# Performance work log

Hardware: AMD Instinct MI355X
Metric: run time of the kernel (lower is better)

The kernel has to match this reference:

```python
import jax, jax.numpy as jnp
import numpy as np

V = 8192        # variants
NREF = 262144   # total ref reads
NALT = 131072   # total alt reads
F_READ = 11     # tensors.NUM_READ_FEATURES
F_INFO = 9      # tensors.NUM_INFO_FEATURES
H = 256         # hidden width
MAX_ALT = 10


def setup_inputs() -> dict:
    key = jax.random.key(0)
    ks = jax.random.split(key, 24)
    p = lambda k, shp: (jax.random.normal(k, shp, dtype=jnp.float32) * 0.05)
    inp = {
        "reads": jax.random.normal(ks[0], (NREF + NALT, F_READ), dtype=jnp.float32),
        "info": jax.random.normal(ks[1], (V, F_INFO), dtype=jnp.float32),
        "ref_seg_ids": jnp.sort(jax.random.randint(ks[2], (NREF,), 0, V, dtype=jnp.int32)),
        "alt_seg_ids": jnp.sort(jax.random.randint(ks[3], (NALT,), 0, V, dtype=jnp.int32)),
        "variant_types": jax.random.randint(ks[4], (V,), 0, 3, dtype=jnp.int32),
        # phi: [F_READ, H, H]
        "phi_W0": p(ks[5], (F_READ, H)), "phi_b0": p(ks[6], (H,)),
        "phi_W1": p(ks[7], (H, H)), "phi_b1": p(ks[8], (H,)),
        # omega: [F_INFO, H]
        "om_W0": p(ks[9], (F_INFO, H)), "om_b0": p(ks[10], (H,)),
        # rho: [3H, H, H]
        "rho_W0": p(ks[11], (3 * H, H)), "rho_b0": p(ks[12], (H,)),
        "rho_W1": p(ks[13], (H, H)), "rho_b1": p(ks[14], (H,)),
        # 3 output MLPs, stacked: [H,H] -> [H,1]
        "out_W1": p(ks[15], (3, H, H)), "out_b1": p(ks[16], (3, H)),
        "out_W2": p(ks[17], (3, H, 1)), "out_b2": p(ks[18], (3, 1)),
        # calibration
        "conf": jnp.sqrt(jnp.arange(0, MAX_ALT + 1, dtype=jnp.float32)),
        "max_logit": jnp.array(10.0, dtype=jnp.float32),
    }
    return inp


def _seg_mean(x, seg_ids, num_segments):
    sums = jax.ops.segment_sum(x, seg_ids, num_segments=num_segments)
    counts = jax.ops.segment_sum(jnp.ones((x.shape[0],), x.dtype), seg_ids, num_segments=num_segments)
    return sums / jnp.maximum(counts, 1.0)[:, None], counts


def reference(reads, info, ref_seg_ids, alt_seg_ids, variant_types,
              phi_W0, phi_b0, phi_W1, phi_b1, om_W0, om_b0,
              rho_W0, rho_b0, rho_W1, rho_b1,
              out_W1, out_b1, out_W2, out_b2, conf, max_logit):
    lrelu = jax.nn.leaky_relu
    # phi MLP (leaky_relu between layers, none after last), then sigmoid
    h = lrelu(reads @ phi_W0 + phi_b0)
    phi_reads = jax.nn.sigmoid(h @ phi_W1 + phi_b1)          # [N, H]
    ref_reads = phi_reads[:NREF]
    alt_reads = phi_reads[NREF:]
    ref_means, _ = _seg_mean(ref_reads, ref_seg_ids, V)       # [V, H]
    alt_means, alt_counts = _seg_mean(alt_reads, alt_seg_ids, V)
    omega_info = jax.nn.sigmoid(info @ om_W0 + om_b0)         # [V, H]
    concat = jnp.concatenate([ref_means, alt_means, omega_info], axis=1)  # [V, 3H]
    agg = lrelu(concat @ rho_W0 + rho_b0) @ rho_W1 + rho_b1   # [V, H]
    # per-variant-type output MLPs, select by variant type
    o = lrelu(jnp.einsum('vd,tde->tve', agg, out_W1) + out_b1[:, None, :])
    outs = (jnp.einsum('tve,teo->tvo', o, out_W2) + out_b2[:, None, :])[:, :, 0]  # [3, V]
    logits = jnp.take_along_axis(outs, variant_types[None, :].astype(jnp.int32), axis=0)[0]
    # calibration
    trunc = jnp.minimum(alt_counts.astype(jnp.int32), MAX_ALT)
    logits = logits * conf[trunc]
    return max_logit * jnp.tanh(logits / max_logit)
```

## Files before the change

### kernel.cpp

```cpp
#include <hip/hip_runtime.h>
#include <hip/hip_bf16.h>
#include <cmath>

#define V 8192
#define NREF 262144
#define NALT 131072
#define NREADS (NREF + NALT)
#define FR 11
#define FI 9
#define HH 256
#define MAX_ALT 10

#define TILE_R 128
#define TILE_V 32

#define HPITCH 264
#define RBPITCH 40
#define CPITCH 776
#define APITCH 264

typedef short bf16x8 __attribute__((ext_vector_type(8)));
typedef float f32x4  __attribute__((ext_vector_type(4)));

__device__ __forceinline__ float lrelu_(float x) {
    return x > 0.0f ? x : 0.01f * x;
}
__device__ __forceinline__ float sigmoidf_(float x) {
    return __builtin_amdgcn_rcpf(1.0f + __expf(-x));
}
__device__ __forceinline__ unsigned short f2bf_(float f) {
    unsigned int u = __float_as_uint(f);
    u += 0x7FFFu + ((u >> 16) & 1u);
    return (unsigned short)(u >> 16);
}
__device__ __forceinline__ float bf2f_(unsigned short b) {
    return __uint_as_float(((unsigned int)b) << 16);
}
__device__ __forceinline__ unsigned int pk2bf_(float a, float b) {
    union { __hip_bfloat162 h2; unsigned int u; } cvt;
    cvt.h2 = __float22bfloat162_rn(make_float2(a, b));
    return cvt.u;
}

__global__ __launch_bounds__(256) void prep_kernel(
    const float* __restrict__ phi_W1, const float* __restrict__ rho_W0,
    const float* __restrict__ rho_W1, const float* __restrict__ out_W1,
    const float* __restrict__ phi_W0,
    unsigned short* __restrict__ w1t_phi, unsigned short* __restrict__ w0t,
    unsigned short* __restrict__ w1rt, unsigned short* __restrict__ whT,
    unsigned short* __restrict__ w0pT, float* __restrict__ zbase)
{
    __shared__ unsigned short sT[32][33];
    const int b = blockIdx.x;
    const int t = threadIdx.x;
    if (b < 512) {
        const float* src; unsigned short* dst; int R, C, bx, by;
        if (b < 64)       { src = phi_W1; dst = w1t_phi; R = 256; C = 256; bx = b & 7; by = b >> 3; }
        else if (b < 256) { int i = b - 64;  src = rho_W0; dst = w0t;  R = 768; C = 256; bx = i & 7; by = i >> 3; }
        else if (b < 320) { int i = b - 256; src = rho_W1; dst = w1rt; R = 256; C = 256; bx = i & 7; by = i >> 3; }
        else              { int i = b - 320; int z = i >> 6; i &= 63;
                            src = out_W1 + (size_t)z * HH * HH; dst = whT + (size_t)z * HH * HH;
                            R = 256; C = 256; bx = i & 7; by = i >> 3; }
        const int tx = t & 31, ty = t >> 5;
        const int r0 = by * 32, c0 = bx * 32;
#pragma unroll
        for (int k = 0; k < 4; k++)
            sT[ty + k * 8][tx] = f2bf_(src[(size_t)(r0 + ty + k * 8) * C + c0 + tx]);
        __syncthreads();
#pragma unroll
        for (int k = 0; k < 4; k++)
            dst[(size_t)(c0 + ty + k * 8) * R + r0 + tx] = sT[tx][ty + k * 8];
    } else if (b < 544) {
        const int idx = (b - 512) * 256 + t;
        const int c = idx >> 5, k = idx & 31;
        unsigned short v = 0;
        if (k < FR) v = f2bf_(phi_W0[k * HH + c]);
        else if (k >= 16 && k < 16 + FR) v = f2bf_(phi_W0[(k - 16) * HH + c]);
        w0pT[idx] = v;
    } else {
        const int n4 = (2 * V * HH + 2 * V) / 4;
        float4 z = {0.f, 0.f, 0.f, 0.f};
        for (int i = (b - 544) * 256 + t; i < n4; i += 1024 * 256)
            ((float4*)zbase)[i] = z;
    }
}

__global__ __launch_bounds__(512, 2) void phi_seg_kernel(
    const float* __restrict__ reads,
    const int* __restrict__ ref_ids, const int* __restrict__ alt_ids,
    const unsigned short* __restrict__ w0pT, const float* __restrict__ b0,
    const unsigned short* __restrict__ w1t, const float* __restrict__ b1,
    float* __restrict__ ref_sums, float* __restrict__ alt_sums,
    int* __restrict__ ref_cnt, int* __restrict__ alt_cnt)
{
    __shared__ __align__(16) unsigned short sH[TILE_R * HPITCH];
    __shared__ __align__(16) unsigned short sRB[TILE_R * RBPITCH];
    __shared__ __align__(16) int sSegL[TILE_R];

    const int t  = threadIdx.x;
    const int r0 = blockIdx.x * TILE_R;
    const bool is_ref = (r0 < NREF);
    const int* seg_ids = is_ref ? ref_ids : alt_ids;
    const int sbase    = is_ref ? r0 : (r0 - NREF);
    float* sums = is_ref ? ref_sums : alt_sums;
    int*   cnts = is_ref ? ref_cnt  : alt_cnt;

    {
        const int row = t & 127, q = t >> 7;
        const float* rp = reads + (size_t)(r0 + row) * FR;
        const int nj = (q & 1) ? 3 : 8;
        const int cb = (q & 1) ? 8 : 0;
        unsigned short o[8];
#pragma unroll
        for (int j = 0; j < 8; j++) o[j] = 0;
        if (q < 2) {
            for (int j = 0; j < nj; j++) o[j] = f2bf_(rp[cb + j]);
        } else {
            for (int j = 0; j < nj; j++) {
                float f = rp[cb + j];
                o[j] = f2bf_(f - bf2f_(f2bf_(f)));
            }
        }
        uint4 pk;
        pk.x = (unsigned int)o[0] | ((unsigned int)o[1] << 16);
        pk.y = (unsigned int)o[2] | ((unsigned int)o[3] << 16);
        pk.z = (unsigned int)o[4] | ((unsigned int)o[5] << 16);
        pk.w = (unsigned int)o[6] | ((unsigned int)o[7] << 16);
        *(uint4*)&sRB[row * RBPITCH + q * 8] = pk;
    }
    if (t < TILE_R) sSegL[t] = seg_ids[sbase + t];
    __syncthreads();

    const int wv   = t >> 6;
    const int lane = t & 63;
    const int lrow = lane & 15;
    const int quad = lane >> 4;

    {
        bf16x8 br[8];
#pragma unroll
        for (int rt = 0; rt < 8; rt++)
            br[rt] = *(const bf16x8*)&sRB[(rt * 16 + lrow) * RBPITCH + quad * 8];

#pragma unroll
        for (int cm = 0; cm < 2; cm++) {
            const bf16x8 aw = *(const bf16x8*)(w0pT + ((wv * 32 + cm * 16 + lrow) << 5) + quad * 8);
            f32x4 c1[8];
#pragma unroll
            for (int rt = 0; rt < 8; rt++)
                c1[rt] = __builtin_amdgcn_mfma_f32_16x16x32_bf16(
                    aw, br[rt], (f32x4){0.f, 0.f, 0.f, 0.f}, 0, 0, 0);

            const float4 bias = *(const float4*)(b0 + wv * 32 + cm * 16 + quad * 4);
#pragma unroll
            for (int rt = 0; rt < 8; rt++) {
                const int r = rt * 16 + lrow;
                uint2 pk;
                pk.x = pk2bf_(lrelu_(c1[rt][0] + bias.x), lrelu_(c1[rt][1] + bias.y));
                pk.y = pk2bf_(lrelu_(c1[rt][2] + bias.z), lrelu_(c1[rt][3] + bias.w));
                *(uint2*)&sH[r * HPITCH + wv * 32 + cm * 16 + quad * 4] = pk;
            }
        }
    }
    __syncthreads();

    f32x4 acc[8][2];
#pragma unroll
    for (int mt = 0; mt < 8; mt++)
#pragma unroll
        for (int nt = 0; nt < 2; nt++)
            acc[mt][nt] = (f32x4){0.f, 0.f, 0.f, 0.f};

#pragma unroll
    for (int kk = 0; kk < 8; kk++) {
        const bf16x8 bn0 = *(const bf16x8*)(w1t + (size_t)(wv * 32 + lrow) * HH + kk * 32 + quad * 8);
        const bf16x8 bn1 = *(const bf16x8*)(w1t + (size_t)(wv * 32 + 16 + lrow) * HH + kk * 32 + quad * 8);
#pragma unroll
        for (int mt = 0; mt < 8; mt++) {
            const bf16x8 am = *(const bf16x8*)&sH[(mt * 16 + lrow) * HPITCH + kk * 32 + quad * 8];
            acc[mt][0] = __builtin_amdgcn_mfma_f32_16x16x32_bf16(am, bn0, acc[mt][0], 0, 0, 0);
            acc[mt][1] = __builtin_amdgcn_mfma_f32_16x16x32_bf16(am, bn1, acc[mt][1], 0, 0, 0);
        }
    }

    const float L2E = 1.44269504f;
#pragma unroll
    for (int nt = 0; nt < 2; nt++) {
        const float nb = -b1[wv * 32 + nt * 16 + lrow] * L2E;
#pragma unroll
        for (int mt = 0; mt < 8; mt++)
#pragma unroll
            for (int r = 0; r < 4; r++) {
                const float e = __builtin_amdgcn_exp2f(fmaf(acc[mt][nt][r], -L2E, nb));
                acc[mt][nt][r] = __builtin_amdgcn_rcpf(1.0f + e);
            }
    }

#pragma unroll
    for (int g = 0; g < 2; g++) {
        const int myseg = seg_ids[sbase + g * 64 + lane];
        const int prev  = __shfl_up(myseg, 1);
        const bool flag = (lane == 0) || (myseg != prev);
        unsigned long long m = __ballot(flag);

        int sgl[4][4];
#pragma unroll
        for (int lm = 0; lm < 4; lm++) {
            const int4 s4 = *(const int4*)&sSegL[g * 64 + lm * 16 + quad * 4];
            sgl[lm][0] = s4.x; sgl[lm][1] = s4.y; sgl[lm][2] = s4.z; sgl[lm][3] = s4.w;
        }

        while (m) {
            const int start = (int)__builtin_ctzll(m);
            m &= m - 1;
            const int end = m ? (int)__builtin_ctzll(m) : 64;
            const int seg = __shfl(myseg, start);
            float* srow = sums + (size_t)seg * HH + wv * 32;

#pragma unroll
            for (int nt = 0; nt < 2; nt++) {
                float s = 0.f;
#pragma unroll
                for (int lm = 0; lm < 4; lm++)
#pragma unroll
                    for (int r = 0; r < 4; r++)
                        s += (sgl[lm][r] == seg) ? acc[g * 4 + lm][nt][r] : 0.f;
                s += __shfl_down(s, 32);
                s += __shfl_down(s, 16);
                if (quad == 0)
                    atomicAdd(&srow[nt * 16 + lrow], s);
            }
            if (t == 0) atomicAdd(&cnts[seg], end - start);
        }
    }
}

__global__ __launch_bounds__(1024, 1) void rho_mfma_kernel(
    const float* __restrict__ info, const int* __restrict__ vtypes,
    const float* __restrict__ om_W0, const float* __restrict__ om_b0,
    const unsigned short* __restrict__ w0t, const float* __restrict__ rho_b0,
    const unsigned short* __restrict__ w1rt, const float* __restrict__ rho_b1,
    const unsigned short* __restrict__ whT, const float* __restrict__ out_b1,
    const float* __restrict__ out_W2, const float* __restrict__ out_b2,
    const float* __restrict__ conf, const float* __restrict__ max_logit,
    const float* __restrict__ ref_sums, const float* __restrict__ alt_sums,
    const int* __restrict__ ref_cnt, const int* __restrict__ alt_cnt,
    float* __restrict__ out)
{
    __shared__ __align__(16) unsigned short sC[TILE_V * CPITCH];
    __shared__ __align__(16) float sInfo[TILE_V][12];
    __shared__ float sRinvR[TILE_V], sRinvA[TILE_V];
    __shared__ float sPart[16][3][TILE_V];

    unsigned short* sA1  = sC;
    unsigned short* sAgg = sC + TILE_V * APITCH;

    const int t  = threadIdx.x;
    const int v0 = blockIdx.x * TILE_V;

    if (t < TILE_V) {
        sRinvR[t] = __builtin_amdgcn_rcpf(fmaxf((float)ref_cnt[v0 + t], 1.0f));
        sRinvA[t] = __builtin_amdgcn_rcpf(fmaxf((float)alt_cnt[v0 + t], 1.0f));
    }
    for (int idx = t; idx < TILE_V * FI; idx += 1024) {
        int i = idx / FI, k = idx - i * FI;
        sInfo[i][k] = info[(size_t)(v0 + i) * FI + k];
    }
    __syncthreads();

    {
        const int c = t & 255, grp = t >> 8;
        float om0r[FI];
#pragma unroll
        for (int k = 0; k < FI; k++) om0r[k] = om_W0[k * HH + c];
        const float omb = om_b0[c];
#pragma unroll
        for (int ii = 0; ii < 8; ii++) {
            const int i = grp * 8 + ii, v = v0 + i;
            float rm = ref_sums[(size_t)v * HH + c] * sRinvR[i];
            float am = alt_sums[(size_t)v * HH + c] * sRinvA[i];
            float a = omb;
#pragma unroll
            for (int k = 0; k < FI; k++) a = fmaf(sInfo[i][k], om0r[k], a);
            sC[i * CPITCH + c]          = f2bf_(rm);
            sC[i * CPITCH + HH + c]     = f2bf_(am);
            sC[i * CPITCH + 2 * HH + c] = f2bf_(sigmoidf_(a));
        }
    }
    __syncthreads();

    const int wv   = t >> 6;
    const int lane = t & 63;
    const int lrow = lane & 15;
    const int quad = lane >> 4;
    const int ncol = wv * 16 + lrow;

    f32x4 p1[2] = {(f32x4){0.f,0.f,0.f,0.f}, (f32x4){0.f,0.f,0.f,0.f}};
#pragma unroll 4
    for (int kk = 0; kk < 24; kk++) {
        bf16x8 a0 = *(const bf16x8*)&sC[lrow * CPITCH + kk * 32 + quad * 8];
        bf16x8 a1 = *(const bf16x8*)&sC[(16 + lrow) * CPITCH + kk * 32 + quad * 8];
        bf16x8 bn = *(const bf16x8*)(w0t + (size_t)ncol * 768 + kk * 32 + quad * 8);
        p1[0] = __builtin_amdgcn_mfma_f32_16x16x32_bf16(a0, bn, p1[0], 0, 0, 0);
        p1[1] = __builtin_amdgcn_mfma_f32_16x16x32_bf16(a1, bn, p1[1], 0, 0, 0);
    }
    __syncthreads();
    {
        const float bb = rho_b0[ncol];
#pragma unroll
        for (int mt = 0; mt < 2; mt++)
#pragma unroll
            for (int r = 0; r < 4; r++) {
                const int row = mt * 16 + quad * 4 + r;
                sA1[row * APITCH + ncol] = f2bf_(lrelu_(p1[mt][r] + bb));
            }
    }
    __syncthreads();

    f32x4 p2[2] = {(f32x4){0.f,0.f,0.f,0.f}, (f32x4){0.f,0.f,0.f,0.f}};
#pragma unroll
    for (int kk = 0; kk < 8; kk++) {
        bf16x8 a0 = *(const bf16x8*)&sA1[lrow * APITCH + kk * 32 + quad * 8];
        bf16x8 a1 = *(const bf16x8*)&sA1[(16 + lrow) * APITCH + kk * 32 + quad * 8];
        bf16x8 bn = *(const bf16x8*)(w1rt + (size_t)ncol * HH + kk * 32 + quad * 8);
        p2[0] = __builtin_amdgcn_mfma_f32_16x16x32_bf16(a0, bn, p2[0], 0, 0, 0);
        p2[1] = __builtin_amdgcn_mfma_f32_16x16x32_bf16(a1, bn, p2[1], 0, 0, 0);
    }
    {
        const float bb = rho_b1[ncol];
#pragma unroll
        for (int mt = 0; mt < 2; mt++)
#pragma unroll
            for (int r = 0; r < 4; r++) {
                const int row = mt * 16 + quad * 4 + r;
                sAgg[row * APITCH + ncol] = f2bf_(p2[mt][r] + bb);
            }
    }
    __syncthreads();

    bf16x8 aF[8][2];
#pragma unroll
    for (int kk = 0; kk < 8; kk++)
#pragma unroll
        for (int mt = 0; mt < 2; mt++)
            aF[kk][mt] = *(const bf16x8*)&sAgg[(mt * 16 + lrow) * APITCH + kk * 32 + quad * 8];

    for (int h = 0; h < 3; h++) {
        f32x4 p3[2] = {(f32x4){0.f,0.f,0.f,0.f}, (f32x4){0.f,0.f,0.f,0.f}};
#pragma unroll
        for (int kk = 0; kk < 8; kk++) {
            bf16x8 bn = *(const bf16x8*)(whT + ((size_t)h * HH + ncol) * HH + kk * 32 + quad * 8);
            p3[0] = __builtin_amdgcn_mfma_f32_16x16x32_bf16(aF[kk][0], bn, p3[0], 0, 0, 0);
            p3[1] = __builtin_amdgcn_mfma_f32_16x16x32_bf16(aF[kk][1], bn, p3[1], 0, 0, 0);
        }
        const float bb = out_b1[h * HH + ncol];
        const float w2 = out_W2[h * HH + ncol];
#pragma unroll
        for (int mt = 0; mt < 2; mt++)
#pragma unroll
            for (int r = 0; r < 4; r++) {
                float v = lrelu_(p3[mt][r] + bb) * w2;
                v += __shfl_down(v, 8);
                v += __shfl_down(v, 4);
                v += __shfl_down(v, 2);
                v += __shfl_down(v, 1);
                if (lrow == 0) sPart[wv][h][mt * 16 + quad * 4 + r] = v;
            }
    }
    __syncthreads();

    if (t < TILE_V) {
        const int v = v0 + t;
        const int ty = vtypes[v];
        float logit = 0.f;
#pragma unroll
        for (int w = 0; w < 16; w++) logit += sPart[w][ty][t];
        logit += out_b2[ty];
        const int tr = min(alt_cnt[v], MAX_ALT);
        logit *= conf[tr];
        const float ml = max_logit[0];
        out[v] = ml * tanhf(logit / ml);
    }
}

extern "C" void kernel_launch(void* const* d_in, const int* in_sizes, int n_in,
                              void* d_out, int out_size, void* d_ws, size_t ws_size,
                              hipStream_t stream) {
    const float* reads    = (const float*)d_in[0];
    const float* info     = (const float*)d_in[1];
    const int*   ref_ids  = (const int*)d_in[2];
    const int*   alt_ids  = (const int*)d_in[3];
    const int*   vtypes   = (const int*)d_in[4];
    const float* phi_W0   = (const float*)d_in[5];
    const float* phi_b0   = (const float*)d_in[6];
    const float* phi_W1   = (const float*)d_in[7];
    const float* phi_b1   = (const float*)d_in[8];
    const float* om_W0    = (const float*)d_in[9];
    const float* om_b0    = (const float*)d_in[10];
    const float* rho_W0   = (const float*)d_in[11];
    const float* rho_b0   = (const float*)d_in[12];
    const float* rho_W1   = (const float*)d_in[13];
    const float* rho_b1   = (const float*)d_in[14];
    const float* out_W1   = (const float*)d_in[15];
    const float* out_b1   = (const float*)d_in[16];
    const float* out_W2   = (const float*)d_in[17];
    const float* out_b2   = (const float*)d_in[18];
    const float* conf     = (const float*)d_in[19];
    const float* max_lg   = (const float*)d_in[20];
    float* out = (float*)d_out;

    float* ref_sums = (float*)d_ws;
    float* alt_sums = ref_sums + (size_t)V * HH;
    int*   ref_cnt  = (int*)(alt_sums + (size_t)V * HH);
    int*   alt_cnt  = ref_cnt + V;
    unsigned short* w1t_phi = (unsigned short*)(alt_cnt + V);
    unsigned short* w0t     = w1t_phi + (size_t)HH * HH;
    unsigned short* w1rt    = w0t + (size_t)HH * 768;
    unsigned short* whT     = w1rt + (size_t)HH * HH;
    unsigned short* w0pT    = whT + (size_t)3 * HH * HH;

    prep_kernel<<<1568, 256, 0, stream>>>(phi_W1, rho_W0, rho_W1, out_W1, phi_W0,
                                          w1t_phi, w0t, w1rt, whT, w0pT,
                                          (float*)d_ws);

    phi_seg_kernel<<<NREADS / TILE_R, 512, 0, stream>>>(
        reads, ref_ids, alt_ids, w0pT, phi_b0, w1t_phi, phi_b1,
        ref_sums, alt_sums, ref_cnt, alt_cnt);

    rho_mfma_kernel<<<V / TILE_V, 1024, 0, stream>>>(
        info, vtypes, om_W0, om_b0, w0t, rho_b0, w1rt, rho_b1,
        whT, out_b1, out_W2, out_b2, conf, max_lg,
        ref_sums, alt_sums, ref_cnt, alt_cnt, out);
}
```

Before: 248.5 us.

## Replace masked per-segment wave reduction with shared-memory transpose and column scans

```diff
diff --git a/kernel.cpp b/kernel.cpp
--- a/kernel.cpp
+++ b/kernel.cpp
@@ -16,8 +16,11 @@
 
 #define HPITCH 264
 #define RBPITCH 40
+#define PTP 136
 #define CPITCH 776
 #define APITCH 264
+
+#define USMEM_BYTES (TILE_R * HPITCH * 2 + TILE_R * RBPITCH * 2)
 
 typedef short bf16x8 __attribute__((ext_vector_type(8)));
 typedef float f32x4  __attribute__((ext_vector_type(4)));
@@ -93,9 +96,12 @@
     float* __restrict__ ref_sums, float* __restrict__ alt_sums,
     int* __restrict__ ref_cnt, int* __restrict__ alt_cnt)
 {
-    __shared__ __align__(16) unsigned short sH[TILE_R * HPITCH];
-    __shared__ __align__(16) unsigned short sRB[TILE_R * RBPITCH];
+    __shared__ __align__(16) unsigned char uSmem[USMEM_BYTES];
     __shared__ __align__(16) int sSegL[TILE_R];
+
+    unsigned short* sH  = (unsigned short*)uSmem;
+    unsigned short* sRB = (unsigned short*)(uSmem + TILE_R * HPITCH * 2);
+    unsigned short* sPT = (unsigned short*)uSmem;
 
     const int t  = threadIdx.x;
     const int r0 = blockIdx.x * TILE_R;
@@ -136,6 +142,8 @@
     const int lrow = lane & 15;
     const int quad = lane >> 4;
 
+    if (t < TILE_R) atomicAdd(&cnts[sSegL[t]], 1);
+
     {
         bf16x8 br[8];
 #pragma unroll
@@ -196,42 +204,42 @@
             }
     }
 
-#pragma unroll
-    for (int g = 0; g < 2; g++) {
-        const int myseg = seg_ids[sbase + g * 64 + lane];
-        const int prev  = __shfl_up(myseg, 1);
-        const bool flag = (lane == 0) || (myseg != prev);
-        unsigned long long m = __ballot(flag);
-
-        int sgl[4][4];
-#pragma unroll
-        for (int lm = 0; lm < 4; lm++) {
-            const int4 s4 = *(const int4*)&sSegL[g * 64 + lm * 16 + quad * 4];
-            sgl[lm][0] = s4.x; sgl[lm][1] = s4.y; sgl[lm][2] = s4.z; sgl[lm][3] = s4.w;
-        }
-
-        while (m) {
-            const int start = (int)__builtin_ctzll(m);
-            m &= m - 1;
-            const int end = m ? (int)__builtin_ctzll(m) : 64;
-            const int seg = __shfl(myseg, start);
-            float* srow = sums + (size_t)seg * HH + wv * 32;
-
-#pragma unroll
-            for (int nt = 0; nt < 2; nt++) {
-                float s = 0.f;
-#pragma unroll
-                for (int lm = 0; lm < 4; lm++)
-#pragma unroll
-                    for (int r = 0; r < 4; r++)
-                        s += (sgl[lm][r] == seg) ? acc[g * 4 + lm][nt][r] : 0.f;
-                s += __shfl_down(s, 32);
-                s += __shfl_down(s, 16);
-                if (quad == 0)
-                    atomicAdd(&srow[nt * 16 + lrow], s);
-            }
-            if (t == 0) atomicAdd(&cnts[seg], end - start);
-        }
+    __syncthreads();
+
+    const int col0 = wv * 32 + lrow;
+    const int col1 = wv * 32 + 16 + lrow;
+#pragma unroll
+    for (int mt = 0; mt < 8; mt++) {
+        uint2 p0, p1;
+        p0.x = pk2bf_(acc[mt][0][0], acc[mt][0][1]);
+        p0.y = pk2bf_(acc[mt][0][2], acc[mt][0][3]);
+        p1.x = pk2bf_(acc[mt][1][0], acc[mt][1][1]);
+        p1.y = pk2bf_(acc[mt][1][2], acc[mt][1][3]);
+        *(uint2*)&sPT[col0 * PTP + mt * 16 + quad * 4] = p0;
+        *(uint2*)&sPT[col1 * PTP + mt * 16 + quad * 4] = p1;
+    }
+    __syncthreads();
+
+    {
+        const int colw = t & 255;
+        const int rb   = (t >> 8) * 64;
+        bf16x8 pcol[8];
+#pragma unroll
+        for (int j = 0; j < 8; j++)
+            pcol[j] = *(const bf16x8*)&sPT[colw * PTP + rb + j * 8];
+
+        int cur = sSegL[rb];
+        float run = 0.f;
+#pragma unroll
+        for (int r = 0; r < 64; r++) {
+            const int s = sSegL[rb + r];
+            if (s != cur) {
+                atomicAdd(&sums[(size_t)cur * HH + colw], run);
+                run = 0.f; cur = s;
+            }
+            run += bf2f_((unsigned short)pcol[r >> 3][r & 7]);
+        }
+        atomicAdd(&sums[(size_t)cur * HH + colw], run);
     }
 }
 
```

Measured after the change: 284.5 us. 1.14x slower.
